# Kernel optimization log

Measured on AMD Instinct MI355X. Metric: run time of the kernel, lower is better.

The kernel has to match this reference:

```python
import jax, jax.numpy as jnp
import numpy as np

EPS = 1e-5

def bn_feat(x, g, b, m, v):
    # BatchNorm1d over (B, F) in eval mode
    return (x - m) / jnp.sqrt(v + EPS) * g + b

def bn_ch(x, g, b, m, v):
    # BatchNorm1d over (B, C, N) in eval mode, per-channel
    inv = (g / jnp.sqrt(v + EPS))[None, :, None]
    return (x - m[None, :, None]) * inv + b[None, :, None]

def conv1(x, w):
    # 1x1 Conv1d without bias: (O,C) x (B,C,N) -> (B,O,N)
    return jnp.einsum('oc,bcn->bon', w, x)


def setup_inputs() -> dict:
    key = jax.random.key(0)
    ks = iter(jax.random.split(key, 48))
    rn = lambda shape, s=0.05: jax.random.normal(next(ks), shape, dtype=jnp.float32) * s
    ru = lambda shape: jax.random.uniform(next(ks), shape, dtype=jnp.float32) + 0.5
    B, M = 32, 2048
    inp = {
        'global_f': jax.random.normal(next(ks), (B, 512, M), dtype=jnp.float32),
        'latent_w': rn((128, 512)), 'latent_b': rn((128,)),
        'token_w': rn((65536, 512)), 'token_b': rn((65536,)),
        'tbn_g': ru((65536,)), 'tbn_b': rn((65536,)), 'tbn_m': rn((65536,)), 'tbn_v': ru((65536,)),
        'q_w': rn((122, 64)), 'qbn_g': ru((122,)), 'qbn_b': rn((122,)), 'qbn_m': rn((122,)), 'qbn_v': ru((122,)),
        'k_w': rn((122, 64)), 'kbn_g': ru((122,)), 'kbn_b': rn((122,)), 'kbn_m': rn((122,)), 'kbn_v': ru((122,)),
        'v_w': rn((122, 64)), 'vbn_g': ru((122,)), 'vbn_b': rn((122,)), 'vbn_m': rn((122,)), 'vbn_v': ru((122,)),
        'f_w': rn((61, 122)), 'fbn_g': ru((61,)), 'fbn_b': rn((61,)), 'fbn_m': rn((61,)), 'fbn_v': ru((61,)),
        'c1_w': rn((256, 61)), 'c1_b': rn((256,)),
        'c2_w': rn((64, 256)), 'c2_b': rn((64,)),
        'c3_w': rn((3, 64)), 'c3_b': rn((3,)),
    }
    return inp


def reference(global_f, latent_w, latent_b, token_w, token_b, tbn_g, tbn_b, tbn_m, tbn_v,
              q_w, qbn_g, qbn_b, qbn_m, qbn_v, k_w, kbn_g, kbn_b, kbn_m, kbn_v,
              v_w, vbn_g, vbn_b, vbn_m, vbn_v, f_w, fbn_g, fbn_b, fbn_m, fbn_v,
              c1_w, c1_b, c2_w, c2_b, c3_w, c3_b):
    B = global_f.shape[0]
    # encoder max-pool: (B,512,M) -> (B,512)
    gfeat = jnp.max(global_f, axis=2)
    # ITSI: latent is computed in torch forward but discarded
    _latent = gfeat @ latent_w.T + latent_b
    tok = gfeat @ token_w.T + token_b                 # (B, 64*1024)
    tok = jax.nn.relu(bn_feat(tok, tbn_g, tbn_b, tbn_m, tbn_v))
    tok = tok.reshape(B, 64, 1024)                    # (B, C=64, N=1024)
    # SelfAttentionUnit (softmax-free)
    q = jax.nn.relu(bn_ch(conv1(tok, q_w), qbn_g, qbn_b, qbn_m, qbn_v))   # (B,122,1024)
    k = jax.nn.relu(bn_ch(conv1(tok, k_w), kbn_g, kbn_b, kbn_m, kbn_v))
    v = jax.nn.relu(bn_ch(conv1(tok, v_w), vbn_g, vbn_b, vbn_m, vbn_v))
    attn = jnp.einsum('bcn,bcm->bnm', q, k)           # Q^T K : (B,1024,1024)
    val = jnp.einsum('bnm,bcm->bcn', attn, v)         # (A V^T)^T : (B,122,1024)
    fused = jax.nn.relu(bn_ch(conv1(val, f_w), fbn_g, fbn_b, fbn_m, fbn_v))  # (B,61,1024)
    h = jax.nn.relu(conv1(fused, c1_w) + c1_b[None, :, None])
    h = jax.nn.relu(conv1(h, c2_w) + c2_b[None, :, None])
    o = jax.nn.sigmoid(conv1(h, c3_w) + c3_b[None, :, None])   # (B,3,1024)
    o = o * 1.0 - 0.5                                  # range_max=0.5: o*0.5*2 - 0.5
    return jnp.transpose(o, (0, 2, 1))                 # (B,1024,3)
```

## Files before the change

### kernel.cpp

```cpp
#include <hip/hip_runtime.h>
#include <float.h>

#define EPS 1e-5f
#define FMA4(A_, W_, T_) { (A_).x += (W_)*(T_).x; (A_).y += (W_)*(T_).y; (A_).z += (W_)*(T_).z; (A_).w += (W_)*(T_).w; }

__global__ __launch_bounds__(256) void k1_maxpool(const float* __restrict__ gf, float* __restrict__ gfeat) {
    int row = blockIdx.x * 4 + (threadIdx.x >> 6);
    int lane = threadIdx.x & 63;
    const float4* p = (const float4*)(gf + (size_t)row * 2048);
    float m = -FLT_MAX;
#pragma unroll
    for (int w = 0; w < 8; ++w) {
        float4 v = p[lane + (w << 6)];
        m = fmaxf(m, fmaxf(fmaxf(v.x, v.y), fmaxf(v.z, v.w)));
    }
#pragma unroll
    for (int off = 32; off >= 1; off >>= 1) m = fmaxf(m, __shfl_xor(m, off));
    if (lane == 0) gfeat[row] = m;
}

__global__ __launch_bounds__(256) void k2_token(
    const float* __restrict__ gfeat, const float* __restrict__ tw, const float* __restrict__ tbias,
    const float* __restrict__ bg, const float* __restrict__ bb,
    const float* __restrict__ bm, const float* __restrict__ bv,
    float* __restrict__ tok) {
    __shared__ __align__(16) float wl[128 * 33];
    __shared__ __align__(16) float gl[32 * 36];
    int tid = threadIdx.x;
    int t0 = blockIdx.x * 128;
    int tx = tid & 7, ty = tid >> 3;
    float4 acc[4];
#pragma unroll
    for (int i = 0; i < 4; ++i) acc[i] = make_float4(0.f, 0.f, 0.f, 0.f);
    for (int k0 = 0; k0 < 512; k0 += 32) {
        if (k0) __syncthreads();
        {
            int r = tid >> 1, h = tid & 1;
            const float* src = tw + (size_t)(t0 + r) * 512 + k0 + h * 16;
            float* dst = wl + r * 33 + h * 16;
#pragma unroll
            for (int q = 0; q < 4; ++q) {
                float4 x = *(const float4*)(src + q * 4);
                dst[q*4+0] = x.x; dst[q*4+1] = x.y; dst[q*4+2] = x.z; dst[q*4+3] = x.w;
            }
            int bq = tid >> 3, kq = tid & 7;
            float4 gx = *(const float4*)(gfeat + bq * 512 + k0 + kq * 4);
            gl[(kq*4+0)*36 + bq] = gx.x;
            gl[(kq*4+1)*36 + bq] = gx.y;
            gl[(kq*4+2)*36 + bq] = gx.z;
            gl[(kq*4+3)*36 + bq] = gx.w;
        }
        __syncthreads();
#pragma unroll
        for (int kk = 0; kk < 32; ++kk) {
            float4 g4 = *(const float4*)(gl + kk * 36 + tx * 4);
#pragma unroll
            for (int i = 0; i < 4; ++i) {
                float a = wl[(ty * 4 + i) * 33 + kk];
                FMA4(acc[i], a, g4);
            }
        }
    }
#pragma unroll
    for (int i = 0; i < 4; ++i) {
        int t = t0 + ty * 4 + i;
        float scale = bg[t] * rsqrtf(bv[t] + EPS);
        float sh = (tbias[t] - bm[t]) * scale + bb[t];
        tok[(size_t)(tx*4+0) * 65536 + t] = fmaxf(acc[i].x * scale + sh, 0.f);
        tok[(size_t)(tx*4+1) * 65536 + t] = fmaxf(acc[i].y * scale + sh, 0.f);
        tok[(size_t)(tx*4+2) * 65536 + t] = fmaxf(acc[i].z * scale + sh, 0.f);
        tok[(size_t)(tx*4+3) * 65536 + t] = fmaxf(acc[i].w * scale + sh, 0.f);
    }
}

__global__ __launch_bounds__(256) void k3_kv(
    const float* __restrict__ tok,
    const float* __restrict__ kw, const float* __restrict__ vw,
    const float* __restrict__ kg, const float* __restrict__ kb, const float* __restrict__ km, const float* __restrict__ kvv,
    const float* __restrict__ vg, const float* __restrict__ vb, const float* __restrict__ vm, const float* __restrict__ vvv,
    float* __restrict__ kbuf, float* __restrict__ vbuf) {
    __shared__ __align__(16) float tokt[64 * 68];
    int tid = threadIdx.x;
    int b = blockIdx.y;
    int n0 = blockIdx.x << 6;
    for (int i = tid; i < 1024; i += 256) {
        int c = i >> 4, q4 = i & 15;
        float4 x = *(const float4*)(tok + (size_t)b * 65536 + c * 1024 + n0 + q4 * 4);
        tokt[(q4*4+0)*68 + c] = x.x;
        tokt[(q4*4+1)*68 + c] = x.y;
        tokt[(q4*4+2)*68 + c] = x.z;
        tokt[(q4*4+3)*68 + c] = x.w;
    }
    int o = tid & 127;
    bool valid = (o < 122);
    float kscl = 0.f, kshf = 0.f, vscl = 0.f, vshf = 0.f;
    if (valid) {
        float s = kg[o] * rsqrtf(kvv[o] + EPS);
        kscl = s; kshf = kb[o] - km[o] * s;
        s = vg[o] * rsqrtf(vvv[o] + EPS);
        vscl = s; vshf = vb[o] - vm[o] * s;
    }
    float4 kwreg[16], vwreg[16];
    {
        const float* kwr = kw + o * 64;
        const float* vwr = vw + o * 64;
#pragma unroll
        for (int c4 = 0; c4 < 16; ++c4) {
            kwreg[c4] = valid ? *(const float4*)(kwr + c4 * 4) : make_float4(0.f,0.f,0.f,0.f);
            vwreg[c4] = valid ? *(const float4*)(vwr + c4 * 4) : make_float4(0.f,0.f,0.f,0.f);
        }
    }
    __syncthreads();
    for (int nn = (tid >> 7); nn < 64; nn += 2) {
        const float* t = tokt + nn * 68;
        float sk = 0.f, sv = 0.f;
#pragma unroll
        for (int c4 = 0; c4 < 16; ++c4) {
            float4 tv = *(const float4*)(t + c4 * 4);
            sk += kwreg[c4].x*tv.x + kwreg[c4].y*tv.y + kwreg[c4].z*tv.z + kwreg[c4].w*tv.w;
            sv += vwreg[c4].x*tv.x + vwreg[c4].y*tv.y + vwreg[c4].z*tv.z + vwreg[c4].w*tv.w;
        }
        size_t base = ((size_t)b * 1024 + n0 + nn) * 128 + o;
        kbuf[base] = fmaxf(sk * kscl + kshf, 0.f);
        vbuf[base] = fmaxf(sv * vscl + vshf, 0.f);
    }
}

__global__ __launch_bounds__(256) void k3_q(
    const float* __restrict__ tok,
    const float* __restrict__ qw,
    const float* __restrict__ qg, const float* __restrict__ qb, const float* __restrict__ qm, const float* __restrict__ qv,
    float* __restrict__ qbuf) {
    __shared__ __align__(16) float tokt[64 * 68];
    int tid = threadIdx.x;
    int b = blockIdx.y;
    int n0 = blockIdx.x << 6;
    for (int i = tid; i < 1024; i += 256) {
        int c = i >> 4, q4 = i & 15;
        float4 x = *(const float4*)(tok + (size_t)b * 65536 + c * 1024 + n0 + q4 * 4);
        tokt[(q4*4+0)*68 + c] = x.x;
        tokt[(q4*4+1)*68 + c] = x.y;
        tokt[(q4*4+2)*68 + c] = x.z;
        tokt[(q4*4+3)*68 + c] = x.w;
    }
    int o = tid & 127;
    bool valid = (o < 122);
    float scl = 0.f, shf = 0.f;
    if (valid) {
        float s = qg[o] * rsqrtf(qv[o] + EPS);
        scl = s; shf = qb[o] - qm[o] * s;
    }
    float4 wreg[16];
    {
        const float* wr = qw + o * 64;
#pragma unroll
        for (int c4 = 0; c4 < 16; ++c4)
            wreg[c4] = valid ? *(const float4*)(wr + c4 * 4) : make_float4(0.f,0.f,0.f,0.f);
    }
    __syncthreads();
    for (int nn = (tid >> 7); nn < 64; nn += 2) {
        const float* t = tokt + nn * 68;
        float s = 0.f;
#pragma unroll
        for (int c4 = 0; c4 < 16; ++c4) {
            float4 tv = *(const float4*)(t + c4 * 4);
            s += wreg[c4].x*tv.x + wreg[c4].y*tv.y + wreg[c4].z*tv.z + wreg[c4].w*tv.w;
        }
        qbuf[((size_t)b * 1024 + n0 + nn) * 128 + o] = fmaxf(s * scl + shf, 0.f);
    }
}

__global__ __launch_bounds__(256) void k4_s(
    const float* __restrict__ kbuf, const float* __restrict__ vbuf,
    float* __restrict__ sp) {
    __shared__ __align__(16) float kl[32 * 128];
    __shared__ __align__(16) float vl[32 * 128];
    int tid = threadIdx.x;
    int b = blockIdx.y, ns = blockIdx.x;
    int tx = tid & 15, ty = tid >> 4;
    float acc[8][8];
#pragma unroll
    for (int i = 0; i < 8; ++i)
#pragma unroll
        for (int j = 0; j < 8; ++j) acc[i][j] = 0.f;
    for (int chunk = 0; chunk < 2; ++chunk) {
        int nb = (ns << 6) + (chunk << 5);
        if (chunk) __syncthreads();
        for (int i = tid; i < 1024; i += 256) {
            int n = i >> 5, q = i & 31;
            size_t src = ((size_t)b * 1024 + nb + n) * 128 + q * 4;
            *(float4*)(kl + n * 128 + q * 4) = *(const float4*)(kbuf + src);
            *(float4*)(vl + n * 128 + q * 4) = *(const float4*)(vbuf + src);
        }
        __syncthreads();
        for (int n = 0; n < 32; ++n) {
            const float* kr = kl + n * 128 + ty * 8;
            const float* vr = vl + n * 128 + tx * 8;
            float4 ka = *(const float4*)(kr),  kb4 = *(const float4*)(kr + 4);
            float4 va = *(const float4*)(vr),  vb4 = *(const float4*)(vr + 4);
            float av[8]  = {ka.x,ka.y,ka.z,ka.w,kb4.x,kb4.y,kb4.z,kb4.w};
            float bvv[8] = {va.x,va.y,va.z,va.w,vb4.x,vb4.y,vb4.z,vb4.w};
#pragma unroll
            for (int i = 0; i < 8; ++i)
#pragma unroll
                for (int j = 0; j < 8; ++j) acc[i][j] += av[i] * bvv[j];
        }
    }
    size_t sbase = ((size_t)(b * 16 + ns)) << 14;
#pragma unroll
    for (int i = 0; i < 8; ++i) {
        int cp = ty * 8 + i;
        *(float4*)(sp + sbase + (cp << 7) + tx * 8)     = make_float4(acc[i][0], acc[i][1], acc[i][2], acc[i][3]);
        *(float4*)(sp + sbase + (cp << 7) + tx * 8 + 4) = make_float4(acc[i][4], acc[i][5], acc[i][6], acc[i][7]);
    }
}

__global__ __launch_bounds__(256) void k4b_reduce(const float* __restrict__ sp, float* __restrict__ spad) {
    int idx = blockIdx.x * 256 + threadIdx.x;
    if (idx >= 32 * 122 * 128) return;
    int c = idx & 127;
    int r = (idx >> 7) % 122;
    int b = idx / (122 * 128);
    float s = 0.f;
    if (c < 122) {
        const float* p = sp + (((size_t)b * 16) << 14) + (r << 7) + c;
#pragma unroll
        for (int q = 0; q < 16; ++q) s += p[(size_t)q << 14];
    }
    spad[idx] = s;
}

__global__ __launch_bounds__(256) void k4c_fold(
    const float* __restrict__ spad, const float* __restrict__ fw,
    const float* __restrict__ fg, const float* __restrict__ fv,
    float* __restrict__ Tt) {
    __shared__ __align__(16) float sl[122 * 128];
    int b = blockIdx.x, tid = threadIdx.x;
    for (int i = tid; i < 3904; i += 256)
        *(float4*)(sl + i * 4) = *(const float4*)(spad + (size_t)b * 15616 + i * 4);
    __syncthreads();
    int o = tid & 63, cpg = tid >> 6;
    if (o < 61) {
        float sc = fg[o] * rsqrtf(fv[o] + EPS);
        const float* fwr = fw + o * 122;
        for (int cp = cpg; cp < 122; cp += 4) {
            const float* sr = sl + cp * 128;
            float s = 0.f;
            for (int c = 0; c < 122; ++c) s += fwr[c] * sr[c];
            Tt[((size_t)b * 122 + cp) * 64 + o] = sc * s;
        }
    }
}

__global__ __launch_bounds__(256) void k5_tail(
    const float* __restrict__ qbuf, const float* __restrict__ Tt,
    const float* __restrict__ fg, const float* __restrict__ fbb,
    const float* __restrict__ fm, const float* __restrict__ fv,
    const float* __restrict__ w1, const float* __restrict__ bb1,
    const float* __restrict__ w2, const float* __restrict__ bb2,
    const float* __restrict__ w3, const float* __restrict__ bb3,
    float* __restrict__ out) {
    __shared__ __align__(16) float lds[7560];
    const int FUS = 0, H1 = 2440, H2 = 6536;
    int tid = threadIdx.x;
    int b = blockIdx.y;
    int n0 = blockIdx.x << 4;
    int nq = tid & 3, og = tid >> 2;
    for (int i = tid; i < 512; i += 256) {
        int n = i >> 5, c4 = i & 31;
        float4 x = *(const float4*)(qbuf + ((size_t)b * 1024 + n0 + n) * 128 + c4 * 4);
        lds[(c4*4+0)*20 + n] = x.x;
        lds[(c4*4+1)*20 + n] = x.y;
        lds[(c4*4+2)*20 + n] = x.z;
        lds[(c4*4+3)*20 + n] = x.w;
    }
    __syncthreads();
    {
        float4 y = make_float4(0.f, 0.f, 0.f, 0.f);
        const bool act = (og < 61);
        if (act) {
            float4 a0 = make_float4(0,0,0,0);
            const float* tb = Tt + (size_t)b * 7808 + og;
            for (int cp = 0; cp < 122; ++cp) {
                float4 tv = *(const float4*)(lds + cp * 20 + nq * 4);
                FMA4(a0, tb[cp << 6], tv);
            }
            float sc = fg[og] * rsqrtf(fv[og] + EPS);
            float sh = fbb[og] - fm[og] * sc;
            y.x = fmaxf(a0.x + sh, 0.f); y.y = fmaxf(a0.y + sh, 0.f);
            y.z = fmaxf(a0.z + sh, 0.f); y.w = fmaxf(a0.w + sh, 0.f);
        }
        __syncthreads();
        if (act) *(float4*)(lds + FUS + og*16 + nq*4) = y;
        __syncthreads();
    }
    {
        float4 a[4];
#pragma unroll
        for (int i = 0; i < 4; ++i) a[i] = make_float4(0,0,0,0);
        for (int c = 0; c < 61; ++c) {
            float4 tv = *(const float4*)(lds + FUS + c*16 + nq*4);
#pragma unroll
            for (int i = 0; i < 4; ++i) {
                float w = w1[(og + (i<<6)) * 61 + c];
                FMA4(a[i], w, tv);
            }
        }
#pragma unroll
        for (int i = 0; i < 4; ++i) {
            int o = og + (i<<6);
            float bias = bb1[o];
            float4 y;
            y.x = fmaxf(a[i].x + bias, 0.f); y.y = fmaxf(a[i].y + bias, 0.f);
            y.z = fmaxf(a[i].z + bias, 0.f); y.w = fmaxf(a[i].w + bias, 0.f);
            *(float4*)(lds + H1 + o*16 + nq*4) = y;
        }
        __syncthreads();
    }
    {
        float4 a0 = make_float4(0,0,0,0);
        const float* w2r = w2 + og * 256;
        for (int c = 0; c < 256; ++c) {
            float4 tv = *(const float4*)(lds + H1 + c*16 + nq*4);
            FMA4(a0, w2r[c], tv);
        }
        float ba = bb2[og];
        float4 y;
        y.x = fmaxf(a0.x + ba, 0.f); y.y = fmaxf(a0.y + ba, 0.f);
        y.z = fmaxf(a0.z + ba, 0.f); y.w = fmaxf(a0.w + ba, 0.f);
        *(float4*)(lds + H2 + og*16 + nq*4) = y;
        __syncthreads();
    }
    if (og < 3) {
        float4 a = make_float4(0,0,0,0);
        const float* w3r = w3 + og * 64;
        for (int c = 0; c < 64; ++c) {
            float4 tv = *(const float4*)(lds + H2 + c*16 + nq*4);
            FMA4(a, w3r[c], tv);
        }
        float bias = bb3[og];
        int nbase = n0 + nq*4;
        out[((size_t)b*1024 + nbase + 0)*3 + og] = 1.f/(1.f+expf(-(a.x+bias))) - 0.5f;
        out[((size_t)b*1024 + nbase + 1)*3 + og] = 1.f/(1.f+expf(-(a.y+bias))) - 0.5f;
        out[((size_t)b*1024 + nbase + 2)*3 + og] = 1.f/(1.f+expf(-(a.z+bias))) - 0.5f;
        out[((size_t)b*1024 + nbase + 3)*3 + og] = 1.f/(1.f+expf(-(a.w+bias))) - 0.5f;
    }
}

extern "C" void kernel_launch(void* const* d_in, const int* in_sizes, int n_in,
                              void* d_out, int out_size, void* d_ws, size_t ws_size,
                              hipStream_t stream) {
    const float* gf      = (const float*)d_in[0];
    const float* token_w = (const float*)d_in[3];
    const float* token_b = (const float*)d_in[4];
    const float* tbn_g   = (const float*)d_in[5];
    const float* tbn_b   = (const float*)d_in[6];
    const float* tbn_m   = (const float*)d_in[7];
    const float* tbn_v   = (const float*)d_in[8];
    const float* q_w = (const float*)d_in[9];
    const float* qg  = (const float*)d_in[10];
    const float* qb  = (const float*)d_in[11];
    const float* qm  = (const float*)d_in[12];
    const float* qv  = (const float*)d_in[13];
    const float* k_w = (const float*)d_in[14];
    const float* kg  = (const float*)d_in[15];
    const float* kb  = (const float*)d_in[16];
    const float* km  = (const float*)d_in[17];
    const float* kv  = (const float*)d_in[18];
    const float* v_w = (const float*)d_in[19];
    const float* vg  = (const float*)d_in[20];
    const float* vb  = (const float*)d_in[21];
    const float* vm  = (const float*)d_in[22];
    const float* vv  = (const float*)d_in[23];
    const float* f_w = (const float*)d_in[24];
    const float* fg  = (const float*)d_in[25];
    const float* fb  = (const float*)d_in[26];
    const float* fm  = (const float*)d_in[27];
    const float* fv  = (const float*)d_in[28];
    const float* c1w = (const float*)d_in[29];
    const float* c1b = (const float*)d_in[30];
    const float* c2w = (const float*)d_in[31];
    const float* c2b = (const float*)d_in[32];
    const float* c3w = (const float*)d_in[33];
    const float* c3b = (const float*)d_in[34];

    float* ws    = (float*)d_ws;
    float* gfeat = ws;
    float* tok   = gfeat + 16384;
    float* kbuf  = tok   + 2097152;
    float* vbuf  = kbuf  + 4194304;
    float* qbuf  = vbuf  + 4194304;
    float* sp    = qbuf  + 4194304;
    float* spad  = sp    + 8388608;
    float* Tt    = spad  + 499712;

    k1_maxpool<<<4096, 256, 0, stream>>>(gf, gfeat);
    k2_token  <<<512, 256, 0, stream>>>(gfeat, token_w, token_b, tbn_g, tbn_b, tbn_m, tbn_v, tok);
    k3_kv     <<<dim3(16, 32), 256, 0, stream>>>(tok, k_w, v_w,
                 kg, kb, km, kv, vg, vb, vm, vv, kbuf, vbuf);
    k3_q      <<<dim3(16, 32), 256, 0, stream>>>(tok, q_w, qg, qb, qm, qv, qbuf);
    k4_s      <<<dim3(16, 32), 256, 0, stream>>>(kbuf, vbuf, sp);
    k4b_reduce<<<1952, 256, 0, stream>>>(sp, spad);
    k4c_fold  <<<32, 256, 0, stream>>>(spad, f_w, fg, fv, Tt);
    k5_tail   <<<dim3(64, 32), 256, 0, stream>>>(qbuf, Tt,
                 fg, fb, fm, fv, c1w, c1b, c2w, c2b, c3w, c3b, (float*)d_out);
}
```

Baseline: 306.3 us.

## Fuse split-K reduce into fold kernel and vectorize tail MLP weight loads

Merges the split-K partial-sum reduction into the fold kernel, so the padded intermediate buffer is no longer written and re-read and there is one fewer launch. The fold now runs on a 4x32 grid instead of 32 blocks, which gives it more parallelism. A prep kernel pads conv1 weights to 64 columns so the tail MLP can read weights with float4 loads and unroll its inner loops by 4. The changes add a small extra launch and reload the fold weights per group.

```diff
diff --git a/kernel.cpp b/kernel.cpp
--- a/kernel.cpp
+++ b/kernel.cpp
@@ -3,6 +3,14 @@
 
 #define EPS 1e-5f
 #define FMA4(A_, W_, T_) { (A_).x += (W_)*(T_).x; (A_).y += (W_)*(T_).y; (A_).z += (W_)*(T_).z; (A_).w += (W_)*(T_).w; }
+
+__global__ __launch_bounds__(256) void k0_prep(const float* __restrict__ w1, float* __restrict__ w1p) {
+    int i = blockIdx.x * 256 + threadIdx.x;
+    if (i < 16384) {
+        int o = i >> 6, c = i & 63;
+        w1p[i] = (c < 61) ? w1[o * 61 + c] : 0.f;
+    }
+}
 
 __global__ __launch_bounds__(256) void k1_maxpool(const float* __restrict__ gf, float* __restrict__ gfeat) {
     int row = blockIdx.x * 4 + (threadIdx.x >> 6);
@@ -215,36 +223,33 @@
     }
 }
 
-__global__ __launch_bounds__(256) void k4b_reduce(const float* __restrict__ sp, float* __restrict__ spad) {
-    int idx = blockIdx.x * 256 + threadIdx.x;
-    if (idx >= 32 * 122 * 128) return;
-    int c = idx & 127;
-    int r = (idx >> 7) % 122;
-    int b = idx / (122 * 128);
-    float s = 0.f;
-    if (c < 122) {
-        const float* p = sp + (((size_t)b * 16) << 14) + (r << 7) + c;
-#pragma unroll
-        for (int q = 0; q < 16; ++q) s += p[(size_t)q << 14];
-    }
-    spad[idx] = s;
-}
-
-__global__ __launch_bounds__(256) void k4c_fold(
-    const float* __restrict__ spad, const float* __restrict__ fw,
+__global__ __launch_bounds__(256) void k4bc_fold(
+    const float* __restrict__ sp, const float* __restrict__ fw,
     const float* __restrict__ fg, const float* __restrict__ fv,
     float* __restrict__ Tt) {
-    __shared__ __align__(16) float sl[122 * 128];
-    int b = blockIdx.x, tid = threadIdx.x;
-    for (int i = tid; i < 3904; i += 256)
-        *(float4*)(sl + i * 4) = *(const float4*)(spad + (size_t)b * 15616 + i * 4);
+    __shared__ __align__(16) float sl[32 * 128];
+    int b = blockIdx.y, g = blockIdx.x;
+    int tid = threadIdx.x;
+    int cp0 = g << 5;
+    for (int i = tid; i < 1024; i += 256) {
+        const float* p = sp + (((size_t)b * 16) << 14) + (size_t)cp0 * 128 + i * 4;
+        float4 acc = make_float4(0.f, 0.f, 0.f, 0.f);
+#pragma unroll
+        for (int q = 0; q < 16; ++q) {
+            float4 x = *(const float4*)(p + ((size_t)q << 14));
+            acc.x += x.x; acc.y += x.y; acc.z += x.z; acc.w += x.w;
+        }
+        *(float4*)(sl + i * 4) = acc;
+    }
     __syncthreads();
     int o = tid & 63, cpg = tid >> 6;
     if (o < 61) {
         float sc = fg[o] * rsqrtf(fv[o] + EPS);
         const float* fwr = fw + o * 122;
-        for (int cp = cpg; cp < 122; cp += 4) {
-            const float* sr = sl + cp * 128;
+        for (int k = cpg; k < 32; k += 4) {
+            int cp = cp0 + k;
+            if (cp >= 122) break;
+            const float* sr = sl + k * 128;
             float s = 0.f;
             for (int c = 0; c < 122; ++c) s += fwr[c] * sr[c];
             Tt[((size_t)b * 122 + cp) * 64 + o] = sc * s;
@@ -256,12 +261,12 @@
     const float* __restrict__ qbuf, const float* __restrict__ Tt,
     const float* __restrict__ fg, const float* __restrict__ fbb,
     const float* __restrict__ fm, const float* __restrict__ fv,
-    const float* __restrict__ w1, const float* __restrict__ bb1,
+    const float* __restrict__ w1p, const float* __restrict__ bb1,
     const float* __restrict__ w2, const float* __restrict__ bb2,
     const float* __restrict__ w3, const float* __restrict__ bb3,
     float* __restrict__ out) {
-    __shared__ __align__(16) float lds[7560];
-    const int FUS = 0, H1 = 2440, H2 = 6536;
+    __shared__ __align__(16) float lds[6144];
+    const int FUS = 0, H1 = 1024, H2 = 5120;
     int tid = threadIdx.x;
     int b = blockIdx.y;
     int n0 = blockIdx.x << 4;
@@ -291,19 +296,29 @@
             y.z = fmaxf(a0.z + sh, 0.f); y.w = fmaxf(a0.w + sh, 0.f);
         }
         __syncthreads();
-        if (act) *(float4*)(lds + FUS + og*16 + nq*4) = y;
+        if (og < 61) *(float4*)(lds + FUS + og*16 + nq*4) = y;
+        if (og >= 61 && og < 64) {
+            *(float4*)(lds + FUS + og*16 + nq*4) = make_float4(0.f,0.f,0.f,0.f);
+        }
         __syncthreads();
     }
     {
         float4 a[4];
 #pragma unroll
         for (int i = 0; i < 4; ++i) a[i] = make_float4(0,0,0,0);
-        for (int c = 0; c < 61; ++c) {
-            float4 tv = *(const float4*)(lds + FUS + c*16 + nq*4);
+#pragma unroll
+        for (int c4 = 0; c4 < 16; ++c4) {
+            float4 t0 = *(const float4*)(lds + FUS + (c4*4+0)*16 + nq*4);
+            float4 t1 = *(const float4*)(lds + FUS + (c4*4+1)*16 + nq*4);
+            float4 t2 = *(const float4*)(lds + FUS + (c4*4+2)*16 + nq*4);
+            float4 t3 = *(const float4*)(lds + FUS + (c4*4+3)*16 + nq*4);
 #pragma unroll
             for (int i = 0; i < 4; ++i) {
-                float w = w1[(og + (i<<6)) * 61 + c];
-                FMA4(a[i], w, tv);
+                float4 w = *(const float4*)(w1p + (og + (i<<6)) * 64 + c4 * 4);
+                FMA4(a[i], w.x, t0);
+                FMA4(a[i], w.y, t1);
+                FMA4(a[i], w.z, t2);
+                FMA4(a[i], w.w, t3);
             }
         }
 #pragma unroll
@@ -320,9 +335,17 @@
     {
         float4 a0 = make_float4(0,0,0,0);
         const float* w2r = w2 + og * 256;
-        for (int c = 0; c < 256; ++c) {
-            float4 tv = *(const float4*)(lds + H1 + c*16 + nq*4);
-            FMA4(a0, w2r[c], tv);
+#pragma unroll 8
+        for (int c4 = 0; c4 < 64; ++c4) {
+            float4 w  = *(const float4*)(w2r + c4 * 4);
+            float4 t0 = *(const float4*)(lds + H1 + (c4*4+0)*16 + nq*4);
+            float4 t1 = *(const float4*)(lds + H1 + (c4*4+1)*16 + nq*4);
+            float4 t2 = *(const float4*)(lds + H1 + (c4*4+2)*16 + nq*4);
+            float4 t3 = *(const float4*)(lds + H1 + (c4*4+3)*16 + nq*4);
+            FMA4(a0, w.x, t0);
+            FMA4(a0, w.y, t1);
+            FMA4(a0, w.z, t2);
+            FMA4(a0, w.w, t3);
         }
         float ba = bb2[og];
         float4 y;
@@ -334,9 +357,17 @@
     if (og < 3) {
         float4 a = make_float4(0,0,0,0);
         const float* w3r = w3 + og * 64;
-        for (int c = 0; c < 64; ++c) {
-            float4 tv = *(const float4*)(lds + H2 + c*16 + nq*4);
-            FMA4(a, w3r[c], tv);
+#pragma unroll
+        for (int c4 = 0; c4 < 16; ++c4) {
+            float4 w  = *(const float4*)(w3r + c4 * 4);
+            float4 t0 = *(const float4*)(lds + H2 + (c4*4+0)*16 + nq*4);
+            float4 t1 = *(const float4*)(lds + H2 + (c4*4+1)*16 + nq*4);
+            float4 t2 = *(const float4*)(lds + H2 + (c4*4+2)*16 + nq*4);
+            float4 t3 = *(const float4*)(lds + H2 + (c4*4+3)*16 + nq*4);
+            FMA4(a, w.x, t0);
+            FMA4(a, w.y, t1);
+            FMA4(a, w.z, t2);
+            FMA4(a, w.w, t3);
         }
         float bias = bb3[og];
         int nbase = n0 + nq*4;
@@ -391,17 +422,17 @@
     float* vbuf  = kbuf  + 4194304;
     float* qbuf  = vbuf  + 4194304;
     float* sp    = qbuf  + 4194304;
-    float* spad  = sp    + 8388608;
-    float* Tt    = spad  + 499712;
-
+    float* Tt    = sp    + 8388608;
+    float* w1p   = Tt    + 249856;
+
+    k0_prep   <<<64, 256, 0, stream>>>(c1w, w1p);
     k1_maxpool<<<4096, 256, 0, stream>>>(gf, gfeat);
     k2_token  <<<512, 256, 0, stream>>>(gfeat, token_w, token_b, tbn_g, tbn_b, tbn_m, tbn_v, tok);
     k3_kv     <<<dim3(16, 32), 256, 0, stream>>>(tok, k_w, v_w,
                  kg, kb, km, kv, vg, vb, vm, vv, kbuf, vbuf);
     k3_q      <<<dim3(16, 32), 256, 0, stream>>>(tok, q_w, qg, qb, qm, qv, qbuf);
     k4_s      <<<dim3(16, 32), 256, 0, stream>>>(kbuf, vbuf, sp);
-    k4b_reduce<<<1952, 256, 0, stream>>>(sp, spad);
-    k4c_fold  <<<32, 256, 0, stream>>>(spad, f_w, fg, fv, Tt);
+    k4bc_fold <<<dim3(4, 32), 256, 0, stream>>>(sp, f_w, fg, fv, Tt);
     k5_tail   <<<dim3(64, 32), 256, 0, stream>>>(qbuf, Tt,
-                 fg, fb, fm, fv, c1w, c1b, c2w, c2b, c3w, c3b, (float*)d_out);
-}
+                 fg, fb, fm, fv, w1p, c1b, c2w, c2b, c3w, c3b, (float*)d_out);
+}
```

Measured after the change: 275.1 us. -10.2%, faster.
